# Kernel optimization log

Hardware: AMD Instinct MI355X
Metric: run time of the kernel (lower is better)

Reference implementation:

```python
import jax, jax.numpy as jnp
import numpy as np

SCALE = 1.0 / np.float32(64.0 ** 0.5)  # module hard-codes sqrt(64), not sqrt(d)


def setup_inputs() -> dict:
    key = jax.random.key(0)
    k1, k2 = jax.random.split(key)
    x = jax.random.normal(k1, (8, 2048, 1024), dtype=jnp.float32)
    kernel = jax.random.normal(k2, (3, 1024, 1024), dtype=jnp.float32) * 0.02
    return {"x": x, "kernel": kernel}


def reference(x, kernel):
    # x: [B, S, D], kernel: [3, D, O]
    wq = jnp.einsum('bsd,do->bso', x, kernel[0])
    wk = jnp.einsum('bsd,do->bso', x, kernel[1])
    wv = jnp.einsum('bsd,do->bso', x, kernel[2])
    scores = jnp.einsum('bqo,bko->bqk', wq, wk) * SCALE  # [B, S, S]
    attn = jax.nn.softmax(scores, axis=-1)
    return jnp.einsum('bqk,bko->bqo', attn, wv)  # [B, S, O]
```

## Files before the change

### kernel.cpp

```cpp
#include <hip/hip_runtime.h>

typedef _Float16 f16;
typedef f16 f16x8 __attribute__((ext_vector_type(8)));
typedef f16 f16x4 __attribute__((ext_vector_type(4)));
typedef float f32x4 __attribute__((ext_vector_type(4)));

#define GLD_LDS16(g, l) __builtin_amdgcn_global_load_lds( \
    (const __attribute__((address_space(1))) void*)(g),   \
    (__attribute__((address_space(3))) void*)(l), 16, 0, 0)

__device__ __forceinline__ void bar() {
    asm volatile("" ::: "memory");
    __builtin_amdgcn_s_barrier();
    asm volatile("" ::: "memory");
}
#define WAIT_VM(n) { asm volatile("s_waitcnt vmcnt(" #n ")" ::: "memory"); \
                     __builtin_amdgcn_sched_barrier(0); }
#define LGKM(n)    { asm volatile("s_waitcnt lgkmcnt(" #n ")" ::: "memory"); \
                     __builtin_amdgcn_sched_barrier(0); }

__global__ __launch_bounds__(256) void cast_f32_f16(const float* __restrict__ x,
                                                    f16* __restrict__ xh) {
    long i = ((long)blockIdx.x * 256 + threadIdx.x) * 8;
    float4 a = *(const float4*)&x[i];
    float4 b = *(const float4*)&x[i + 4];
    f16x8 v;
    v[0] = (f16)a.x; v[1] = (f16)a.y; v[2] = (f16)a.z; v[3] = (f16)a.w;
    v[4] = (f16)b.x; v[5] = (f16)b.y; v[6] = (f16)b.z; v[7] = (f16)b.w;
    *(f16x8*)&xh[i] = v;
}

__global__ __launch_bounds__(256) void cast_transpose_1k(const float* __restrict__ Wi,
                                                         f16* __restrict__ WTi) {
    __shared__ float tile[64][65];
    const int d0 = blockIdx.y * 64;
    const int o0 = blockIdx.x * 64;
    const int t = threadIdx.x;
#pragma unroll
    for (int j = 0; j < 4; ++j) {
        int idx = t + j * 256;
        int r = idx >> 4;
        int c4 = (idx & 15) * 4;
        float4 v = *(const float4*)&Wi[(long)(d0 + r) * 1024 + o0 + c4];
        tile[r][c4 + 0] = v.x; tile[r][c4 + 1] = v.y;
        tile[r][c4 + 2] = v.z; tile[r][c4 + 3] = v.w;
    }
    __syncthreads();
#pragma unroll
    for (int j = 0; j < 2; ++j) {
        int idx = t + j * 256;
        int ol = idx >> 3;
        int c8 = (idx & 7) * 8;
        f16x8 v;
#pragma unroll
        for (int e = 0; e < 8; ++e) v[e] = (f16)tile[c8 + e][ol];
        *(f16x8*)&WTi[(long)(o0 + ol) * 1024 + d0 + c8] = v;
    }
}

__global__ __launch_bounds__(256, 2)
void gemm_mp(const f16* __restrict__ A, const f16* __restrict__ B,
             f16* __restrict__ C) {
    __shared__ f16x8 ls[2][2][4][128];
    const int tid = threadIdx.x;
    const int lane = tid & 63;
    const int wave = tid >> 6;
    const int wm = wave >> 1;
    const int wn = wave & 1;
    const long m_base = (long)blockIdx.y * 128;
    const long n_base = (long)blockIdx.x * 128;

    const int i1 = tid + 256;
    const int kb0 = tid >> 7, r0 = tid & 127;
    const int kb1 = i1 >> 7, r1 = i1 & 127;
    const f16* gA0 = A + (m_base + r0) * 1024L + kb0 * 8;
    const f16* gA1 = A + (m_base + r1) * 1024L + kb1 * 8;
    const f16* gB0 = B + (n_base + r0) * 1024L + kb0 * 8;
    const f16* gB1 = B + (n_base + r1) * 1024L + kb1 * 8;

    auto stage = [&](int buf, int k0) {
        GLD_LDS16(gA0 + k0, &ls[buf][0][kb0][r0]);
        GLD_LDS16(gA1 + k0, &ls[buf][0][kb1][r1]);
        GLD_LDS16(gB0 + k0, &ls[buf][1][kb0][r0]);
        GLD_LDS16(gB1 + k0, &ls[buf][1][kb1][r1]);
    };

    f32x4 acc[4][4];
#pragma unroll
    for (int i = 0; i < 4; ++i)
#pragma unroll
        for (int j = 0; j < 4; ++j) acc[i][j] = (f32x4){0.f, 0.f, 0.f, 0.f};

    stage(0, 0);
    WAIT_VM(0);
    bar();
    int cur = 0;
    const int kb = lane >> 4;
    const int fr = lane & 15;
    for (int t = 0; t < 32; ++t) {
        if (t + 1 < 32) stage(cur ^ 1, (t + 1) << 5);
        f16x8 af[4], bf[4];
#pragma unroll
        for (int mi = 0; mi < 4; ++mi) af[mi] = ls[cur][0][kb][wm * 64 + mi * 16 + fr];
#pragma unroll
        for (int ni = 0; ni < 4; ++ni) bf[ni] = ls[cur][1][kb][wn * 64 + ni * 16 + fr];
#pragma unroll
        for (int mi = 0; mi < 4; ++mi)
#pragma unroll
            for (int ni = 0; ni < 4; ++ni)
                acc[mi][ni] = __builtin_amdgcn_mfma_f32_16x16x32_f16(
                    af[mi], bf[ni], acc[mi][ni], 0, 0, 0);
        WAIT_VM(0);
        bar();
        cur ^= 1;
    }
    const int rq = lane >> 4;
#pragma unroll
    for (int mi = 0; mi < 4; ++mi) {
        long r0_ = m_base + wm * 64 + mi * 16 + rq * 4;
#pragma unroll
        for (int ni = 0; ni < 4; ++ni) {
            long c = n_base + wn * 64 + ni * 16 + fr;
#pragma unroll
            for (int j = 0; j < 4; ++j)
                C[(r0_ + j) * 1024L + c] = (f16)acc[mi][ni][j];
        }
    }
}

template <int MODE, int TILES>
__global__ __launch_bounds__(512, 2)
void gemm256(const f16* __restrict__ A, const f16* __restrict__ B,
             void* __restrict__ Cv, const float* __restrict__ dinv,
             float* __restrict__ psum,
             int lda, int ldb, int K,
             long sA, long sB, long sC, int ldc, float scale) {
    extern __shared__ __align__(16) char smem[];
    const int tid = threadIdx.x;
    const int lane = tid & 63;
    const int wave = tid >> 6;
    const int wm = wave >> 2;
    const int wn = wave & 3;
    const int z = blockIdx.z;

    const int o_ = blockIdx.x + gridDim.x * blockIdx.y;
    const int nwg = gridDim.x * gridDim.y;
    const int sw = (o_ & 7) * (nwg >> 3) + (o_ >> 3);
    const int bxb = sw % gridDim.x;
    const int by = sw / gridDim.x;

    const long m_base = (long)by * 256;
    const f16* Ab = A + (long)z * sA;
    const f16* Bb = B + (long)z * sB;

    const int c_r0 = tid >> 3;
    const int c_col = ((tid & 7) * 8) ^ ((c_r0 & 7) << 3);
    const long oA0 = (m_base + c_r0) * (long)lda + c_col;
    const long oA1 = oA0 + 64L * lda;
    long oB0 = ((long)(bxb * TILES) * 256 + c_r0) * (long)ldb + c_col;
    long oB1 = oB0 + 64L * ldb;

#define ST_A0(bf_, kt_) { long k0_ = (long)(kt_) * 64; \
    char* d_ = smem + (bf_) * 65536 + tid * 16; \
    GLD_LDS16(Ab + oA0 + k0_, d_); GLD_LDS16(Ab + oA1 + k0_, d_ + 8192); }
#define ST_A1(bf_, kt_) { long k0_ = (long)(kt_) * 64 + 128L * lda; \
    char* d_ = smem + (bf_) * 65536 + 16384 + tid * 16; \
    GLD_LDS16(Ab + oA0 + k0_, d_); GLD_LDS16(Ab + oA1 + k0_, d_ + 8192); }
#define ST_B0(bf_, kt_) { long k0_ = (long)(kt_) * 64; \
    char* d_ = smem + (bf_) * 65536 + 32768 + tid * 16; \
    GLD_LDS16(Bb + oB0 + k0_, d_); GLD_LDS16(Bb + oB1 + k0_, d_ + 8192); }
#define ST_B1(bf_, kt_) { long k0_ = (long)(kt_) * 64 + 128L * ldb; \
    char* d_ = smem + (bf_) * 65536 + 49152 + tid * 16; \
    GLD_LDS16(Bb + oB0 + k0_, d_); GLD_LDS16(Bb + oB1 + k0_, d_ + 8192); }

    const int fr = lane & 15;
    const int rq = lane >> 4;
    const int cs0 = (rq * 16) ^ ((lane & 7) << 4);
    const int cs1 = cs0 ^ 64;
    const int aoff = wm * 16384 + fr * 128;
    const int boff = 32768 + (wn >> 1) * 16384 + (wn & 1) * 8192 + fr * 128;

    const int NT = K >> 6;

    ST_B0(0, 0); ST_B1(0, 0); ST_A0(0, 0); ST_A1(0, 0);
    WAIT_VM(4);
    ST_B0(1, 1); ST_B1(1, 1); ST_A0(1, 1);
    WAIT_VM(6);
    bar();

    for (int tt = 0; tt < TILES; ++tt) {
        const long n_base = (long)(bxb * TILES + tt) * 256;

        f32x4 acc[8][4];
#pragma unroll
        for (int i = 0; i < 8; ++i)
#pragma unroll
            for (int j = 0; j < 4; ++j) acc[i][j] = (f32x4){0.f, 0.f, 0.f, 0.f};

        for (int j = 0; j < NT; ++j) {
            char* bufb = smem + (j & 1) * 65536;
            const char* Ap = bufb + aoff;
            const char* Bp = bufb + boff;
            f16x8 af[4][2], bf[4][2];

#pragma unroll
            for (int i = 0; i < 4; ++i) {
                af[i][0] = *(const f16x8*)(Ap + i * 2048 + cs0);
                af[i][1] = *(const f16x8*)(Ap + i * 2048 + cs1);
            }
            __builtin_amdgcn_sched_barrier(0);
#pragma unroll
            for (int ni = 0; ni < 2; ++ni) {
                bf[ni][0] = *(const f16x8*)(Bp + ni * 2048 + cs0);
                bf[ni][1] = *(const f16x8*)(Bp + ni * 2048 + cs1);
            }
            __builtin_amdgcn_sched_barrier(0);
#pragma unroll
            for (int ni = 2; ni < 4; ++ni) {
                bf[ni][0] = *(const f16x8*)(Bp + ni * 2048 + cs0);
                bf[ni][1] = *(const f16x8*)(Bp + ni * 2048 + cs1);
            }
            if (j + 1 < NT) ST_A1((j + 1) & 1, j + 1);
            bar();
            LGKM(4);
            __builtin_amdgcn_s_setprio(1);
#pragma unroll
            for (int ks = 0; ks < 2; ++ks)
#pragma unroll
                for (int i = 0; i < 4; ++i)
#pragma unroll
                    for (int n = 0; n < 2; ++n)
                        acc[i][n] = __builtin_amdgcn_mfma_f32_16x16x32_f16(
                            af[i][ks], bf[n][ks], acc[i][n], 0, 0, 0);
            __builtin_amdgcn_s_setprio(0);
            bar();

            LGKM(0);
            if (j + 2 < NT) ST_B0(j & 1, j + 2);
            bar();
            __builtin_amdgcn_s_setprio(1);
#pragma unroll
            for (int ks = 0; ks < 2; ++ks)
#pragma unroll
                for (int i = 0; i < 4; ++i)
#pragma unroll
                    for (int n = 0; n < 2; ++n)
                        acc[i][2 + n] = __builtin_amdgcn_mfma_f32_16x16x32_f16(
                            af[i][ks], bf[2 + n][ks], acc[i][2 + n], 0, 0, 0);
            __builtin_amdgcn_s_setprio(0);
            bar();

#pragma unroll
            for (int i = 0; i < 4; ++i) {
                af[i][0] = *(const f16x8*)(Ap + (4 + i) * 2048 + cs0);
                af[i][1] = *(const f16x8*)(Ap + (4 + i) * 2048 + cs1);
            }
            if (j + 2 < NT) ST_B1(j & 1, j + 2);
            bar();
            LGKM(0);
            __builtin_amdgcn_s_setprio(1);
#pragma unroll
            for (int ks = 0; ks < 2; ++ks)
#pragma unroll
                for (int i = 0; i < 4; ++i)
#pragma unroll
                    for (int n = 0; n < 2; ++n)
                        acc[4 + i][n] = __builtin_amdgcn_mfma_f32_16x16x32_f16(
                            af[i][ks], bf[n][ks], acc[4 + i][n], 0, 0, 0);
            __builtin_amdgcn_s_setprio(0);
            bar();

            if (j + 2 < NT) {
                ST_A0(j & 1, j + 2);
                WAIT_VM(6);
            } else if (j + 1 < NT) {
                WAIT_VM(0);
            }
            bar();
            __builtin_amdgcn_s_setprio(1);
#pragma unroll
            for (int ks = 0; ks < 2; ++ks)
#pragma unroll
                for (int i = 0; i < 4; ++i)
#pragma unroll
                    for (int n = 0; n < 2; ++n)
                        acc[4 + i][2 + n] = __builtin_amdgcn_mfma_f32_16x16x32_f16(
                            af[i][ks], bf[2 + n][ks], acc[4 + i][2 + n], 0, 0, 0);
            __builtin_amdgcn_s_setprio(0);
            bar();
        }

        if (tt + 1 < TILES) {
            oB0 = ((long)(bxb * TILES + tt + 1) * 256 + c_r0) * (long)ldb + c_col;
            oB1 = oB0 + 64L * ldb;
            ST_B0(0, 0); ST_B1(0, 0); ST_A0(0, 0); ST_A1(0, 0);
            ST_B0(1, 1); ST_B1(1, 1); ST_A0(1, 1);
        }

        if constexpr (MODE == 0) {
            f16* C = (f16*)Cv + (long)z * sC;
            float p[8][4];
#pragma unroll
            for (int mi = 0; mi < 8; ++mi)
#pragma unroll
                for (int jj = 0; jj < 4; ++jj) p[mi][jj] = 0.f;
#pragma unroll
            for (int mi = 0; mi < 8; ++mi) {
                long r0 = m_base + wm * 128 + mi * 16 + rq * 4;
#pragma unroll
                for (int ni = 0; ni < 4; ++ni) {
                    long c = n_base + wn * 64 + ni * 16 + fr;
#pragma unroll
                    for (int jj = 0; jj < 4; ++jj) {
                        float e = exp2f(acc[mi][ni][jj] * scale - 5.77078016f);
                        C[(r0 + jj) * (long)ldc + c] = (f16)e;
                        p[mi][jj] += e;
                    }
                }
            }
#pragma unroll
            for (int mi = 0; mi < 8; ++mi)
#pragma unroll
                for (int jj = 0; jj < 4; ++jj)
#pragma unroll
                    for (int o = 8; o; o >>= 1)
                        p[mi][jj] += __shfl_xor(p[mi][jj], o);
            float* wsum = (float*)smem;
            if (fr == 0) {
#pragma unroll
                for (int mi = 0; mi < 8; ++mi)
#pragma unroll
                    for (int jj = 0; jj < 4; ++jj)
                        wsum[wn * 256 + wm * 128 + mi * 16 + rq * 4 + jj] = p[mi][jj];
            }
            bar();
            if (tid < 256) {
                float s = wsum[tid] + wsum[256 + tid] + wsum[512 + tid] + wsum[768 + tid];
                psum[((long)z * 2048 + m_base + tid) * 8 + (int)(n_base >> 8)] = s;
            }
        } else {
#pragma unroll
            for (int mi = 0; mi < 8; ++mi) {
                long r0 = m_base + wm * 128 + mi * 16 + rq * 4;
#pragma unroll
                for (int ni = 0; ni < 4; ++ni) {
                    long c = n_base + wn * 64 + ni * 16 + fr;
                    if constexpr (MODE == 2) {
                        float* C = (float*)Cv + (long)z * sC;
#pragma unroll
                        for (int jj = 0; jj < 4; ++jj)
                            C[(r0 + jj) * (long)ldc + c] =
                                acc[mi][ni][jj] * dinv[(long)z * 2048 + r0 + jj];
                    } else {
                        if (c < 1024) {
                            f16* T = (f16*)Cv;
#pragma unroll
                            for (int jj = 0; jj < 4; ++jj)
                                T[(r0 + jj) * 1024L + c] = (f16)acc[mi][ni][jj];
                        } else {
                            f16* VT = (f16*)((char*)Cv + 67108864);
                            long o = c - 1024;
                            long b = r0 >> 11;
                            long s = r0 & 2047;
                            f16x4 v;
#pragma unroll
                            for (int jj = 0; jj < 4; ++jj) v[jj] = (f16)acc[mi][ni][jj];
                            *(f16x4*)&VT[b * 2097152L + o * 2048L + s] = v;
                        }
                    }
                }
            }
        }

        if (tt + 1 < TILES) {
            WAIT_VM(6);
            bar();
        }
    }
#undef ST_A0
#undef ST_A1
#undef ST_B0
#undef ST_B1
}

__global__ __launch_bounds__(256) void reduce_dinv(const float* __restrict__ psum,
                                                   float* __restrict__ dinv) {
    int r = blockIdx.x * 256 + threadIdx.x;
    float4 a = *(const float4*)&psum[(long)r * 8];
    float4 b = *(const float4*)&psum[(long)r * 8 + 4];
    dinv[r] = 1.f / (a.x + a.y + a.z + a.w + b.x + b.y + b.z + b.w);
}

extern "C" void kernel_launch(void* const* d_in, const int* in_sizes, int n_in,
                              void* d_out, int out_size, void* d_ws, size_t ws_size,
                              hipStream_t stream) {
    const float* x = (const float*)d_in[0];
    const float* w = (const float*)d_in[1];
    float* out = (float*)d_out;
    char* ws = (char*)d_ws;

    f16* th  = (f16*)(ws + 0);
    f16* xh  = (f16*)(ws + 33554432);
    f16* vt  = (f16*)(ws + 67108864);
    char* spB = ws + 100663296;
    f16* whq = (f16*)(spB);
    f16* whk = (f16*)(spB + 2097152);
    f16* bTV = (f16*)(spB + 4194304);
    f16* sp  = (f16*)(spB);
    float* dinv = (float*)(ws + 0);
    float* psum = (float*)d_out;

    cast_f32_f16<<<1024, 256, 0, stream>>>(w, whq);
    cast_transpose_1k<<<dim3(16, 16), 256, 0, stream>>>(w + 2097152, bTV + 1048576);
    cast_f32_f16<<<8192, 256, 0, stream>>>(x, xh);

    gemm_mp<<<dim3(8, 8), 256, 0, stream>>>(whk, whq, bTV);

    gemm256<4, 2><<<dim3(4, 64, 1), 512, 131072, stream>>>(
        xh, bTV, ws, nullptr, nullptr, 1024, 1024, 1024, 0L, 0L, 0L, 0, 1.0f);

    gemm256<0, 1><<<dim3(8, 8, 8), 512, 131072, stream>>>(
        th, xh, sp, nullptr, psum, 1024, 1024, 1024,
        2097152L, 2097152L, 4194304L, 2048, 0.125f * 1.44269504f);

    reduce_dinv<<<64, 256, 0, stream>>>(psum, dinv);

    gemm256<2, 1><<<dim3(4, 8, 8), 512, 131072, stream>>>(
        sp, vt, out, dinv, nullptr, 2048, 2048, 2048,
        4194304L, 2097152L, 2097152L, 1024, 1.0f);
}
```

Before: 292.3 us.

## Add XCD-aware tile swizzle and M-direction multi-tile for score GEMM

Replaces the workgroup remapping with a parameterized XCD-aware rectangular swizzle (RW x RH block regions per XCD) so blocks on the same XCD share A/B panels in L2. The score GEMM now computes two 256-row tiles per workgroup along M, reusing the same B panel and halving the grid. The row-sum scratch moves past the double buffer into extra LDS so prefetching the next tile does not clobber it. The extra LDS per block may lower occupancy for the score kernel, and fewer workgroups could leave CUs underused.

```diff
diff --git a/kernel.cpp b/kernel.cpp
--- a/kernel.cpp
+++ b/kernel.cpp
@@ -128,7 +128,7 @@
     }
 }
 
-template <int MODE, int TILES>
+template <int MODE, int TILES, int TDIR, int RW, int RH>
 __global__ __launch_bounds__(512, 2)
 void gemm256(const f16* __restrict__ A, const f16* __restrict__ B,
              void* __restrict__ Cv, const float* __restrict__ dinv,
@@ -144,20 +144,23 @@
     const int z = blockIdx.z;
 
     const int o_ = blockIdx.x + gridDim.x * blockIdx.y;
-    const int nwg = gridDim.x * gridDim.y;
-    const int sw = (o_ & 7) * (nwg >> 3) + (o_ >> 3);
-    const int bxb = sw % gridDim.x;
-    const int by = sw / gridDim.x;
-
-    const long m_base = (long)by * 256;
+    const int xcd = o_ & 7;
+    const int idx = o_ >> 3;
+    const int nrbx = gridDim.x / RW;
+    const int bx_s = (xcd % nrbx) * RW + (idx % RW);
+    const int by_s = (xcd / nrbx) * RH + (idx / RW);
+
+    const int tile_m0 = (TDIR == 1) ? by_s * TILES : by_s;
+    const int tile_n0 = (TDIR == 0) ? bx_s * TILES : bx_s;
+
     const f16* Ab = A + (long)z * sA;
     const f16* Bb = B + (long)z * sB;
 
     const int c_r0 = tid >> 3;
     const int c_col = ((tid & 7) * 8) ^ ((c_r0 & 7) << 3);
-    const long oA0 = (m_base + c_r0) * (long)lda + c_col;
-    const long oA1 = oA0 + 64L * lda;
-    long oB0 = ((long)(bxb * TILES) * 256 + c_r0) * (long)ldb + c_col;
+    long oA0 = ((long)tile_m0 * 256 + c_r0) * (long)lda + c_col;
+    long oA1 = oA0 + 64L * lda;
+    long oB0 = ((long)tile_n0 * 256 + c_r0) * (long)ldb + c_col;
     long oB1 = oB0 + 64L * ldb;
 
 #define ST_A0(bf_, kt_) { long k0_ = (long)(kt_) * 64; \
@@ -189,7 +192,8 @@
     bar();
 
     for (int tt = 0; tt < TILES; ++tt) {
-        const long n_base = (long)(bxb * TILES + tt) * 256;
+        const long m_base = (long)((TDIR == 1) ? tile_m0 + tt : tile_m0) * 256;
+        const long n_base = (long)((TDIR == 0) ? tile_n0 + tt : tile_n0) * 256;
 
         f32x4 acc[8][4];
 #pragma unroll
@@ -291,8 +295,13 @@
         }
 
         if (tt + 1 < TILES) {
-            oB0 = ((long)(bxb * TILES + tt + 1) * 256 + c_r0) * (long)ldb + c_col;
-            oB1 = oB0 + 64L * ldb;
+            if (TDIR == 0) {
+                oB0 = ((long)(tile_n0 + tt + 1) * 256 + c_r0) * (long)ldb + c_col;
+                oB1 = oB0 + 64L * ldb;
+            } else {
+                oA0 = ((long)(tile_m0 + tt + 1) * 256 + c_r0) * (long)lda + c_col;
+                oA1 = oA0 + 64L * lda;
+            }
             ST_B0(0, 0); ST_B1(0, 0); ST_A0(0, 0); ST_A1(0, 0);
             ST_B0(1, 1); ST_B1(1, 1); ST_A0(1, 1);
         }
@@ -325,7 +334,7 @@
 #pragma unroll
                     for (int o = 8; o; o >>= 1)
                         p[mi][jj] += __shfl_xor(p[mi][jj], o);
-            float* wsum = (float*)smem;
+            float* wsum = (float*)(smem + 131072);
             if (fr == 0) {
 #pragma unroll
                 for (int mi = 0; mi < 8; ++mi)
@@ -416,16 +425,16 @@
 
     gemm_mp<<<dim3(8, 8), 256, 0, stream>>>(whk, whq, bTV);
 
-    gemm256<4, 2><<<dim3(4, 64, 1), 512, 131072, stream>>>(
+    gemm256<4, 2, 0, 4, 8><<<dim3(4, 64, 1), 512, 131072, stream>>>(
         xh, bTV, ws, nullptr, nullptr, 1024, 1024, 1024, 0L, 0L, 0L, 0, 1.0f);
 
-    gemm256<0, 1><<<dim3(8, 8, 8), 512, 131072, stream>>>(
+    gemm256<0, 2, 1, 2, 2><<<dim3(8, 4, 8), 512, 135168, stream>>>(
         th, xh, sp, nullptr, psum, 1024, 1024, 1024,
         2097152L, 2097152L, 4194304L, 2048, 0.125f * 1.44269504f);
 
     reduce_dinv<<<64, 256, 0, stream>>>(psum, dinv);
 
-    gemm256<2, 1><<<dim3(4, 8, 8), 512, 131072, stream>>>(
+    gemm256<2, 1, 1, 2, 2><<<dim3(4, 8, 8), 512, 131072, stream>>>(
         sp, vt, out, dinv, nullptr, 2048, 2048, 2048,
         4194304L, 2097152L, 2097152L, 1024, 1.0f);
 }
```

Measured after the change: 295.5 us. No clear change (+1.1%).
